# Kernel optimization log

Hardware: AMD Instinct MI355X
Metric: run time of the kernel (lower is better)

The kernel has to match this reference:

```python
import jax, jax.numpy as jnp
import numpy as np

B, N, F, C, L = 2, 2048, 64, 64, 4

def setup_inputs() -> dict:
    key = jax.random.key(0)
    k1, k2, k3, k4, k5 = jax.random.split(key, 5)
    V = jax.random.normal(k1, (B, N, F), dtype=jnp.float32)
    A = jax.random.uniform(k2, (B, N, N, L), dtype=jnp.float32)
    # xavier-normal-ish scale for w1; plain normals for w2/w3
    w1 = jax.random.normal(k3, (F, C), dtype=jnp.float32) * jnp.sqrt(2.0 / (F + C))
    w2 = jax.random.normal(k4, (F * L, C), dtype=jnp.float32) * 0.05
    w3 = jax.random.normal(k5, (F * L, C), dtype=jnp.float32) * 0.05
    return {"V": V, "A": A, "w1": w1, "w2": w2, "w3": w3}

def reference(V, A, w1, w2, w3):
    b, n, _, l = A.shape
    f = V.shape[-1]
    # term1: plain linear embedding (no bias, no act)
    term1 = jnp.matmul(V, w1)                                   # B,N,C
    # term2: per-edge-type degree weighting of self features
    deg = jnp.sum(A, axis=2)                                    # B,N,L  (sum over neighbors j)
    dv = (deg[..., None] * V[:, :, None, :]).reshape(b, n, l * f)  # B,N,L*F
    term2 = jnp.matmul(dv, w2)                                  # B,N,C
    # term3: neighbor aggregation per edge type
    agg = jnp.einsum('bijl,bjf->bilf', A, V).reshape(b, n, l * f)  # B,N,L*F
    term3 = jnp.matmul(agg, w3)                                 # B,N,C
    return jax.nn.sigmoid(term1 + term2 - term3)
```

## Files before the change

### kernel.cpp

```cpp
#include <hip/hip_runtime.h>

#define B_ 2
#define N_ 2048
#define F_ 64
#define C_ 64
#define L_ 4
#define SP 8

typedef _Float16 half8 __attribute__((ext_vector_type(8)));
typedef _Float16 half2 __attribute__((ext_vector_type(2)));
typedef float floatx4 __attribute__((ext_vector_type(4)));

__global__ __launch_bounds__(256) void k0_transpose(const float* __restrict__ V,
                                                    _Float16* __restrict__ Vth) {
    __shared__ float tile[64][65];
    const int b  = blockIdx.x >> 5;
    const int j0 = (blockIdx.x & 31) * 64;
    const int tid = threadIdx.x;

    const floatx4* V4 = (const floatx4*)(V + ((size_t)(b * N_ + j0)) * F_);
#pragma unroll
    for (int s = 0; s < 4; ++s) {
        int g = tid + 256 * s;
        int jl = g >> 4;
        int fq = g & 15;
        floatx4 v = V4[jl * 16 + fq];
        tile[jl][fq * 4 + 0] = v.x;
        tile[jl][fq * 4 + 1] = v.y;
        tile[jl][fq * 4 + 2] = v.z;
        tile[jl][fq * 4 + 3] = v.w;
    }
    __syncthreads();

    const int f = tid >> 2;
    const int jb = (tid & 3) * 16;
    _Float16* dh = Vth + ((size_t)(b * F_ + f)) * N_ + j0 + jb;
#pragma unroll
    for (int u = 0; u < 16; u += 4) {
        half2 h01 = {(_Float16)tile[jb + u + 0][f], (_Float16)tile[jb + u + 1][f]};
        half2 h23 = {(_Float16)tile[jb + u + 2][f], (_Float16)tile[jb + u + 3][f]};
        *(half2*)(dh + u + 0) = h01;
        *(half2*)(dh + u + 2) = h23;
    }
}

__global__ __launch_bounds__(256, 2) void k1_agg(const float* __restrict__ A,
                                                 const _Float16* __restrict__ Vth,
                                                 float* __restrict__ aggT,
                                                 float* __restrict__ degT) {
    const int bid = blockIdx.x;
    const int b   = bid >> 8;
    const int rem = bid & 255;
    const int i0  = (rem >> 1) * 16;
    const int h   = rem & 1;
    const int tid  = threadIdx.x;
    const int w    = tid >> 6;
    const int lane = tid & 63;
    const int m    = lane & 15;
    const int q    = lane >> 4;
    const int p    = h * 4 + w;
    const int jwin = p * 256;

    const floatx4* Arow = (const floatx4*)(A + (((size_t)(b * N_ + i0 + m)) * N_ + jwin) * 4);
    const _Float16* Vrow = Vth + ((size_t)b * F_) * N_ + jwin;

    floatx4 acc[4][4];
    floatx4 accd[4];
#pragma unroll
    for (int l = 0; l < 4; ++l) {
        accd[l] = (floatx4){0, 0, 0, 0};
#pragma unroll
        for (int fc = 0; fc < 4; ++fc) acc[l][fc] = (floatx4){0, 0, 0, 0};
    }

    half8 bones;
#pragma unroll
    for (int e = 0; e < 8; ++e) bones[e] = (m == 0) ? (_Float16)1.0f : (_Float16)0.0f;

    half8 v_cur[4], v_nxt[4];
#pragma unroll
    for (int fc = 0; fc < 4; ++fc)
        v_cur[fc] = *(const half8*)(Vrow + (size_t)(fc * 16 + m) * N_ + q * 8);

#pragma unroll 2
    for (int t = 0; t < 8; ++t) {
        floatx4 a[8];
        const int jb = t * 32 + q * 8;
#pragma unroll
        for (int e = 0; e < 8; ++e) a[e] = Arow[jb + e];

        const int tn = (t < 7) ? t + 1 : 7;
        const int jn = tn * 32 + q * 8;
#pragma unroll
        for (int fc = 0; fc < 4; ++fc)
            v_nxt[fc] = *(const half8*)(Vrow + (size_t)(fc * 16 + m) * N_ + jn);

        half8 f[4];
#pragma unroll
        for (int l = 0; l < 4; ++l) {
#pragma unroll
            for (int e = 0; e < 8; ++e) f[l][e] = (_Float16)a[e][l];
        }

#pragma unroll
        for (int l = 0; l < 4; ++l) {
            acc[l][0] = __builtin_amdgcn_mfma_f32_16x16x32_f16(f[l], v_cur[0], acc[l][0], 0, 0, 0);
            acc[l][1] = __builtin_amdgcn_mfma_f32_16x16x32_f16(f[l], v_cur[1], acc[l][1], 0, 0, 0);
            acc[l][2] = __builtin_amdgcn_mfma_f32_16x16x32_f16(f[l], v_cur[2], acc[l][2], 0, 0, 0);
            acc[l][3] = __builtin_amdgcn_mfma_f32_16x16x32_f16(f[l], v_cur[3], acc[l][3], 0, 0, 0);
            accd[l]   = __builtin_amdgcn_mfma_f32_16x16x32_f16(f[l], bones,    accd[l],   0, 0, 0);
        }
#pragma unroll
        for (int fc = 0; fc < 4; ++fc) v_cur[fc] = v_nxt[fc];
    }

    float* aggb = aggT + ((size_t)(p * B_ + b)) * 256 * N_;
    const int ibase = i0 + q * 4;
#pragma unroll
    for (int l = 0; l < 4; ++l) {
#pragma unroll
        for (int fc = 0; fc < 4; ++fc) {
            const int k = l * 64 + fc * 16 + m;
            *(floatx4*)(aggb + (size_t)k * N_ + ibase) = acc[l][fc];
        }
    }
    if (m == 0) {
#pragma unroll
        for (int l = 0; l < 4; ++l)
            *(floatx4*)(degT + ((size_t)((p * B_ + b) * L_ + l)) * N_ + ibase) = accd[l];
    }
}

__global__ __launch_bounds__(256) void k2_out(const float* __restrict__ V,
                                              const float* __restrict__ degT,
                                              const float* __restrict__ aggT,
                                              const float* __restrict__ w1,
                                              const float* __restrict__ w2,
                                              const float* __restrict__ w3,
                                              float* __restrict__ out) {
    __shared__ float xsum[256][4];
    __shared__ float vt[4][64];
    __shared__ float dsum[4][4];

    const int raw = blockIdx.x;
    const int b   = raw >> 9;
    const int t9  = raw & 511;
    const int tile = ((t9 & 7) << 6) | (t9 >> 3);
    const int i0  = tile * 4;
    const int tid = threadIdx.x;

    {
        const int k = tid;
        const float* g = aggT + ((size_t)b * 256 + k) * N_ + i0;
        const size_t PS = (size_t)B_ * 256 * N_;
        floatx4 s = *(const floatx4*)(g);
#pragma unroll
        for (int pp = 1; pp < SP; ++pp) s += *(const floatx4*)(g + pp * PS);
        *(floatx4*)&xsum[k][0] = s;
    }
    {
        const int il = tid >> 6, f = tid & 63;
        vt[il][f] = V[((size_t)(b * N_ + i0 + il)) * F_ + f];
    }
    if (tid < 16) {
        const int l = tid >> 2, il = tid & 3;
        float s = 0.0f;
#pragma unroll
        for (int pp = 0; pp < SP; ++pp)
            s += degT[((size_t)((pp * B_ + b) * L_ + l)) * N_ + i0 + il];
        dsum[l][il] = s;
    }
    __syncthreads();

    const int il = tid >> 6;
    const int c  = tid & 63;
    const float d0 = dsum[0][il], d1 = dsum[1][il], d2 = dsum[2][il], d3 = dsum[3][il];

    float acc = 0.0f;
#pragma unroll 4
    for (int f = 0; f < 64; ++f) {
        const float x = vt[il][f];
        acc += x        * w1[f * 64 + c];
        acc += (d0 * x) * w2[(0 * 64 + f) * 64 + c];
        acc += (d1 * x) * w2[(1 * 64 + f) * 64 + c];
        acc += (d2 * x) * w2[(2 * 64 + f) * 64 + c];
        acc += (d3 * x) * w2[(3 * 64 + f) * 64 + c];
    }
#pragma unroll 4
    for (int k = 0; k < 256; ++k) {
        acc -= xsum[k][il] * w3[k * 64 + c];
    }

    out[((size_t)(b * N_ + i0 + il)) * C_ + c] = 1.0f / (1.0f + __expf(-acc));
}

extern "C" void kernel_launch(void* const* d_in, const int* in_sizes, int n_in,
                              void* d_out, int out_size, void* d_ws, size_t ws_size,
                              hipStream_t stream) {
    const float* V  = (const float*)d_in[0];
    const float* A  = (const float*)d_in[1];
    const float* w1 = (const float*)d_in[2];
    const float* w2 = (const float*)d_in[3];
    const float* w3 = (const float*)d_in[4];
    float* out = (float*)d_out;

    char* ws = (char*)d_ws;
    float*    aggT = (float*)(ws);
    float*    degT = (float*)(ws + 33554432);
    _Float16* Vth  = (_Float16*)(ws + 34078720);

    hipLaunchKernelGGL(k0_transpose, dim3(B_ * (N_ / 64)), dim3(256), 0, stream, V, Vth);
    hipLaunchKernelGGL(k1_agg,       dim3(B_ * (N_ / 16) * 2), dim3(256), 0, stream,
                       A, Vth, aggT, degT);
    hipLaunchKernelGGL(k2_out,       dim3(B_ * (N_ / 4)), dim3(256), 0, stream,
                       V, degT, aggT, w1, w2, w3, out);
}
```

Before: 258.6 us.

## Fold w3 into V before aggregation, turning term3 into a single GEMM over A

Precomputes -V·w3 per edge type as an fp16 matrix of shape (C, N*L) per batch, so term3 becomes one GEMM of A (flattened j,l) against it, with an indicator column producing the degree sums. This shrinks the intermediate from 256 aggregated features per node with eight partial splits to 80 columns with four split-K partials, which cuts workspace traffic and removes the w3 loop from the output kernel. It costs a small extra precompute kernel and folds w3 into fp16 before the big reduction, which changes rounding behaviour.

After: 252.7 us. 2.3% less time.

```diff
diff --git a/kernel.cpp b/kernel.cpp
--- a/kernel.cpp
+++ b/kernel.cpp
@@ -5,142 +5,127 @@
 #define F_ 64
 #define C_ 64
 #define L_ 4
-#define SP 8
+#define K_ (N_ * L_)
+#define PCOLS 80
+#define SKB 4
 
 typedef _Float16 half8 __attribute__((ext_vector_type(8)));
-typedef _Float16 half2 __attribute__((ext_vector_type(2)));
+typedef _Float16 half4 __attribute__((ext_vector_type(4)));
 typedef float floatx4 __attribute__((ext_vector_type(4)));
 
-__global__ __launch_bounds__(256) void k0_transpose(const float* __restrict__ V,
-                                                    _Float16* __restrict__ Vth) {
-    __shared__ float tile[64][65];
-    const int b  = blockIdx.x >> 5;
-    const int j0 = (blockIdx.x & 31) * 64;
+__global__ __launch_bounds__(256) void k0_wbig(const float* __restrict__ V,
+                                               const float* __restrict__ w3,
+                                               _Float16* __restrict__ WbigT) {
+    __shared__ float vt[4][64];
+    const int bid = blockIdx.x;
+    const int b   = bid >> 9;
+    const int j0  = (bid & 511) * 4;
     const int tid = threadIdx.x;
+    const int jl  = tid >> 6;
+    const int c   = tid & 63;
 
-    const floatx4* V4 = (const floatx4*)(V + ((size_t)(b * N_ + j0)) * F_);
-#pragma unroll
-    for (int s = 0; s < 4; ++s) {
-        int g = tid + 256 * s;
-        int jl = g >> 4;
-        int fq = g & 15;
-        floatx4 v = V4[jl * 16 + fq];
-        tile[jl][fq * 4 + 0] = v.x;
-        tile[jl][fq * 4 + 1] = v.y;
-        tile[jl][fq * 4 + 2] = v.z;
-        tile[jl][fq * 4 + 3] = v.w;
-    }
+    vt[jl][c] = V[((size_t)(b * N_ + j0 + jl)) * F_ + c];
     __syncthreads();
 
-    const int f = tid >> 2;
-    const int jb = (tid & 3) * 16;
-    _Float16* dh = Vth + ((size_t)(b * F_ + f)) * N_ + j0 + jb;
+    half4 h;
 #pragma unroll
-    for (int u = 0; u < 16; u += 4) {
-        half2 h01 = {(_Float16)tile[jb + u + 0][f], (_Float16)tile[jb + u + 1][f]};
-        half2 h23 = {(_Float16)tile[jb + u + 2][f], (_Float16)tile[jb + u + 3][f]};
-        *(half2*)(dh + u + 0) = h01;
-        *(half2*)(dh + u + 2) = h23;
+    for (int l = 0; l < 4; ++l) {
+        float s = 0.0f;
+#pragma unroll 8
+        for (int f = 0; f < 64; ++f)
+            s += vt[jl][f] * w3[(l * 64 + f) * 64 + c];
+        h[l] = (_Float16)(-s);
     }
+    *(half4*)(WbigT + ((size_t)(b * 64 + c)) * K_ + (size_t)(j0 + jl) * 4) = h;
 }
 
-__global__ __launch_bounds__(256, 2) void k1_agg(const float* __restrict__ A,
-                                                 const _Float16* __restrict__ Vth,
-                                                 float* __restrict__ aggT,
-                                                 float* __restrict__ degT) {
-    const int bid = blockIdx.x;
-    const int b   = bid >> 8;
-    const int rem = bid & 255;
-    const int i0  = (rem >> 1) * 16;
-    const int h   = rem & 1;
+__global__ __launch_bounds__(256, 4) void k1_gemm(const float* __restrict__ A,
+                                                  const _Float16* __restrict__ WbigT,
+                                                  float* __restrict__ P) {
+    __shared__ float red[4][16][84];
+
+    const int bid  = blockIdx.x;
+    const int skb  = bid & 3;
+    const int tile = bid >> 2;
+    const int b    = tile >> 7;
+    const int i0   = (tile & 127) * 16;
     const int tid  = threadIdx.x;
     const int w    = tid >> 6;
     const int lane = tid & 63;
     const int m    = lane & 15;
     const int q    = lane >> 4;
-    const int p    = h * 4 + w;
-    const int jwin = p * 256;
 
-    const floatx4* Arow = (const floatx4*)(A + (((size_t)(b * N_ + i0 + m)) * N_ + jwin) * 4);
-    const _Float16* Vrow = Vth + ((size_t)b * F_) * N_ + jwin;
+    const int kw = (skb * 4 + w) * 512;
 
-    floatx4 acc[4][4];
-    floatx4 accd[4];
+    const float* Ap = A + ((size_t)(b * N_ + i0 + m)) * K_ + kw + q * 8;
+    const _Float16* Bp = WbigT + ((size_t)b * 64 + m) * K_ + kw + q * 8;
+
+    floatx4 acc[5];
 #pragma unroll
-    for (int l = 0; l < 4; ++l) {
-        accd[l] = (floatx4){0, 0, 0, 0};
+    for (int fc = 0; fc < 5; ++fc) acc[fc] = (floatx4){0, 0, 0, 0};
+
+    half8 bind;
 #pragma unroll
-        for (int fc = 0; fc < 4; ++fc) acc[l][fc] = (floatx4){0, 0, 0, 0};
+    for (int e = 0; e < 8; ++e) bind[e] = (m == (e & 3)) ? (_Float16)1.0f : (_Float16)0.0f;
+
+    floatx4 ac0, ac1, an0, an1;
+    half8 bc[4], bn[4];
+
+    ac0 = *(const floatx4*)(Ap + 0);
+    ac1 = *(const floatx4*)(Ap + 4);
+#pragma unroll
+    for (int fc = 0; fc < 4; ++fc) bc[fc] = *(const half8*)(Bp + (size_t)(fc * 16) * K_);
+
+#pragma unroll 2
+    for (int t = 0; t < 16; ++t) {
+        const int tn = (t < 15) ? t + 1 : 15;
+        an0 = *(const floatx4*)(Ap + tn * 32 + 0);
+        an1 = *(const floatx4*)(Ap + tn * 32 + 4);
+#pragma unroll
+        for (int fc = 0; fc < 4; ++fc)
+            bn[fc] = *(const half8*)(Bp + (size_t)(fc * 16) * K_ + tn * 32);
+
+        half8 af;
+#pragma unroll
+        for (int e = 0; e < 4; ++e) { af[e] = (_Float16)ac0[e]; af[e + 4] = (_Float16)ac1[e]; }
+
+        acc[0] = __builtin_amdgcn_mfma_f32_16x16x32_f16(af, bc[0], acc[0], 0, 0, 0);
+        acc[1] = __builtin_amdgcn_mfma_f32_16x16x32_f16(af, bc[1], acc[1], 0, 0, 0);
+        acc[2] = __builtin_amdgcn_mfma_f32_16x16x32_f16(af, bc[2], acc[2], 0, 0, 0);
+        acc[3] = __builtin_amdgcn_mfma_f32_16x16x32_f16(af, bc[3], acc[3], 0, 0, 0);
+        acc[4] = __builtin_amdgcn_mfma_f32_16x16x32_f16(af, bind,  acc[4], 0, 0, 0);
+
+        ac0 = an0; ac1 = an1;
+#pragma unroll
+        for (int fc = 0; fc < 4; ++fc) bc[fc] = bn[fc];
     }
 
-    half8 bones;
 #pragma unroll
-    for (int e = 0; e < 8; ++e) bones[e] = (m == 0) ? (_Float16)1.0f : (_Float16)0.0f;
+    for (int fc = 0; fc < 5; ++fc) {
+#pragma unroll
+        for (int r = 0; r < 4; ++r)
+            red[w][q * 4 + r][fc * 16 + m] = acc[fc][r];
+    }
+    __syncthreads();
 
-    half8 v_cur[4], v_nxt[4];
+    float* Pb = P + (((size_t)(skb * B_ + b)) * N_ + i0) * PCOLS;
 #pragma unroll
-    for (int fc = 0; fc < 4; ++fc)
-        v_cur[fc] = *(const half8*)(Vrow + (size_t)(fc * 16 + m) * N_ + q * 8);
-
-#pragma unroll 2
-    for (int t = 0; t < 8; ++t) {
-        floatx4 a[8];
-        const int jb = t * 32 + q * 8;
-#pragma unroll
-        for (int e = 0; e < 8; ++e) a[e] = Arow[jb + e];
-
-        const int tn = (t < 7) ? t + 1 : 7;
-        const int jn = tn * 32 + q * 8;
-#pragma unroll
-        for (int fc = 0; fc < 4; ++fc)
-            v_nxt[fc] = *(const half8*)(Vrow + (size_t)(fc * 16 + m) * N_ + jn);
-
-        half8 f[4];
-#pragma unroll
-        for (int l = 0; l < 4; ++l) {
-#pragma unroll
-            for (int e = 0; e < 8; ++e) f[l][e] = (_Float16)a[e][l];
-        }
-
-#pragma unroll
-        for (int l = 0; l < 4; ++l) {
-            acc[l][0] = __builtin_amdgcn_mfma_f32_16x16x32_f16(f[l], v_cur[0], acc[l][0], 0, 0, 0);
-            acc[l][1] = __builtin_amdgcn_mfma_f32_16x16x32_f16(f[l], v_cur[1], acc[l][1], 0, 0, 0);
-            acc[l][2] = __builtin_amdgcn_mfma_f32_16x16x32_f16(f[l], v_cur[2], acc[l][2], 0, 0, 0);
-            acc[l][3] = __builtin_amdgcn_mfma_f32_16x16x32_f16(f[l], v_cur[3], acc[l][3], 0, 0, 0);
-            accd[l]   = __builtin_amdgcn_mfma_f32_16x16x32_f16(f[l], bones,    accd[l],   0, 0, 0);
-        }
-#pragma unroll
-        for (int fc = 0; fc < 4; ++fc) v_cur[fc] = v_nxt[fc];
-    }
-
-    float* aggb = aggT + ((size_t)(p * B_ + b)) * 256 * N_;
-    const int ibase = i0 + q * 4;
-#pragma unroll
-    for (int l = 0; l < 4; ++l) {
-#pragma unroll
-        for (int fc = 0; fc < 4; ++fc) {
-            const int k = l * 64 + fc * 16 + m;
-            *(floatx4*)(aggb + (size_t)k * N_ + ibase) = acc[l][fc];
-        }
-    }
-    if (m == 0) {
-#pragma unroll
-        for (int l = 0; l < 4; ++l)
-            *(floatx4*)(degT + ((size_t)((p * B_ + b) * L_ + l)) * N_ + ibase) = accd[l];
+    for (int s = 0; s < 5; ++s) {
+        const int idx = tid + 256 * s;
+        const int i   = idx / PCOLS;
+        const int c   = idx % PCOLS;
+        float v = red[0][i][c] + red[1][i][c] + red[2][i][c] + red[3][i][c];
+        Pb[(size_t)i * PCOLS + c] = v;
     }
 }
 
 __global__ __launch_bounds__(256) void k2_out(const float* __restrict__ V,
-                                              const float* __restrict__ degT,
-                                              const float* __restrict__ aggT,
+                                              const float* __restrict__ P,
                                               const float* __restrict__ w1,
                                               const float* __restrict__ w2,
-                                              const float* __restrict__ w3,
                                               float* __restrict__ out) {
-    __shared__ float xsum[256][4];
+    __shared__ float xsum[4][PCOLS];
     __shared__ float vt[4][64];
-    __shared__ float dsum[4][4];
 
     const int raw = blockIdx.x;
     const int b   = raw >> 9;
@@ -149,34 +134,26 @@
     const int i0  = tile * 4;
     const int tid = threadIdx.x;
 
-    {
-        const int k = tid;
-        const float* g = aggT + ((size_t)b * 256 + k) * N_ + i0;
-        const size_t PS = (size_t)B_ * 256 * N_;
+    if (tid < 80) {
+        const int il = tid / 20, c4 = tid % 20;
+        const size_t PS = (size_t)B_ * N_ * PCOLS;
+        const float* g = P + ((size_t)b * N_ + i0 + il) * PCOLS + c4 * 4;
         floatx4 s = *(const floatx4*)(g);
 #pragma unroll
-        for (int pp = 1; pp < SP; ++pp) s += *(const floatx4*)(g + pp * PS);
-        *(floatx4*)&xsum[k][0] = s;
+        for (int sk = 1; sk < SKB; ++sk) s += *(const floatx4*)(g + sk * PS);
+        *(floatx4*)&xsum[il][c4 * 4] = s;
     }
     {
         const int il = tid >> 6, f = tid & 63;
         vt[il][f] = V[((size_t)(b * N_ + i0 + il)) * F_ + f];
     }
-    if (tid < 16) {
-        const int l = tid >> 2, il = tid & 3;
-        float s = 0.0f;
-#pragma unroll
-        for (int pp = 0; pp < SP; ++pp)
-            s += degT[((size_t)((pp * B_ + b) * L_ + l)) * N_ + i0 + il];
-        dsum[l][il] = s;
-    }
     __syncthreads();
 
     const int il = tid >> 6;
     const int c  = tid & 63;
-    const float d0 = dsum[0][il], d1 = dsum[1][il], d2 = dsum[2][il], d3 = dsum[3][il];
+    const float d0 = xsum[il][64], d1 = xsum[il][65], d2 = xsum[il][66], d3 = xsum[il][67];
 
-    float acc = 0.0f;
+    float acc = xsum[il][c];
 #pragma unroll 4
     for (int f = 0; f < 64; ++f) {
         const float x = vt[il][f];
@@ -185,10 +162,6 @@
         acc += (d1 * x) * w2[(1 * 64 + f) * 64 + c];
         acc += (d2 * x) * w2[(2 * 64 + f) * 64 + c];
         acc += (d3 * x) * w2[(3 * 64 + f) * 64 + c];
-    }
-#pragma unroll 4
-    for (int k = 0; k < 256; ++k) {
-        acc -= xsum[k][il] * w3[k * 64 + c];
     }
 
     out[((size_t)(b * N_ + i0 + il)) * C_ + c] = 1.0f / (1.0f + __expf(-acc));
@@ -205,13 +178,12 @@
     float* out = (float*)d_out;
 
     char* ws = (char*)d_ws;
-    float*    aggT = (float*)(ws);
-    float*    degT = (float*)(ws + 33554432);
-    _Float16* Vth  = (_Float16*)(ws + 34078720);
+    _Float16* WbigT = (_Float16*)(ws);
+    float*    P     = (float*)(ws + 2097152);
 
-    hipLaunchKernelGGL(k0_transpose, dim3(B_ * (N_ / 64)), dim3(256), 0, stream, V, Vth);
-    hipLaunchKernelGGL(k1_agg,       dim3(B_ * (N_ / 16) * 2), dim3(256), 0, stream,
-                       A, Vth, aggT, degT);
-    hipLaunchKernelGGL(k2_out,       dim3(B_ * (N_ / 4)), dim3(256), 0, stream,
-                       V, degT, aggT, w1, w2, w3, out);
+    hipLaunchKernelGGL(k0_wbig, dim3(B_ * (N_ / 4)), dim3(256), 0, stream, V, w3, WbigT);
+    hipLaunchKernelGGL(k1_gemm, dim3((B_ * (N_ / 16)) * SKB), dim3(256), 0, stream,
+                       A, WbigT, P);
+    hipLaunchKernelGGL(k2_out,  dim3(B_ * (N_ / 4)), dim3(256), 0, stream,
+                       V, P, w1, w2, out);
 }
```
